# Kernel tuning notes

Measured on AMD Instinct MI355X. Metric: run time of the kernel, lower is better.

Reference implementation:

```python
import jax, jax.numpy as jnp
import numpy as np

N = 8192
K = 30


def setup_inputs() -> dict:
    key = jax.random.key(0)
    k1, k2, k3 = jax.random.split(key, 3)
    estimate = jax.random.normal(k1, (N, K), dtype=jnp.float32)
    event_time = jax.random.uniform(k2, (N,), dtype=jnp.float32) * 30.0
    event = (jax.random.uniform(k3, (N,)) < 0.7).astype(jnp.float32)
    target = jnp.stack([event_time, event], axis=1)  # [N, 2]
    intervals = (jnp.arange(K, dtype=jnp.float32) + 0.5)  # midpoints per init_kwargs
    return {"estimate": estimate, "target": target, "intervals": intervals}


def reference(estimate, target, intervals):
    event_time = target[:, 0]
    event = target[:, 1] != 0
    # hazard -> survival via exclusive cumprod (pad with 1 at the front)
    hazard = jax.nn.sigmoid(estimate)                       # [N, K]
    surv = jnp.cumprod(1.0 - hazard, axis=-1)               # inclusive cumprod
    surv_prev = jnp.concatenate(
        [jnp.ones_like(surv[..., :1]), surv[..., :-1]], axis=-1
    )                                                       # S(t_{k-1}), exclusive
    pdf = hazard * surv_prev                                # [N, K]
    mrl = jnp.sum(intervals * pdf, axis=-1)                 # [N]
    # comparable pairs: i has an event and t_i < t_j
    comparable = (event_time[:, None] < event_time[None, :]) & event[:, None]
    diff = mrl[:, None] - mrl[None, :]                      # [N, N]
    cnt = jnp.sum(comparable).astype(diff.dtype)
    return jnp.sum(jnp.where(comparable, diff, 0.0)) / cnt
```

## Files before the change

kernel.cpp:

```cpp
#include <hip/hip_runtime.h>
#include <math.h>

constexpr int N     = 8192;
constexpr int K     = 30;
constexpr int TPB   = 1024;
constexpr int NI    = N / TPB;
constexpr int NJ    = 32;
constexpr int JSPAN = N / NJ;
constexpr int NBLK  = NI * NJ;
constexpr int MB    = 128;
constexpr int FTPB  = 256;


__global__ void mrl_kernel(const float* __restrict__ est,
                           const float* __restrict__ intervals,
                           float* __restrict__ mrl) {
    __shared__ float s_est[MB * K];

    const int tid  = threadIdx.x;
    const int row0 = blockIdx.x * MB;

    const float2* src = (const float2*)(est + (size_t)row0 * K);
    float2* dst = (float2*)s_est;
#pragma unroll
    for (int t = 0; t < K / 2; ++t)
        dst[t * MB + tid] = src[t * MB + tid];
    __syncthreads();

    const float* e = s_est + tid * K;
    double sp = 1.0, m = 0.0;
#pragma unroll
    for (int k = 0; k < K; ++k) {
        float hf = 1.0f / (1.0f + __expf(-e[k]));
        double h = (double)hf;
        m += (double)intervals[k] * h * sp;
        sp *= (1.0 - h);
    }
    mrl[row0 + tid] = (float)m;
}

__global__ void pair_kernel(const float* __restrict__ target,
                            const float* __restrict__ mrl,
                            double* __restrict__ pnum,
                            int* __restrict__ pcnt) {
    __shared__ __align__(16) float s_t[JSPAN];
    __shared__ __align__(16) float s_m[JSPAN];
    __shared__ double r_num[TPB];
    __shared__ int    r_cnt[TPB];

    const int tid = threadIdx.x;
    const int bid = blockIdx.x;
    const int ib  = bid >> 5;
    const int js  = bid & (NJ - 1);
    const int i   = ib * TPB + tid;

    const float2 ti2 = ((const float2*)target)[i];
    const float  ti  = ti2.x;
    const bool   ei  = (ti2.y != 0.0f);
    const float  mi  = mrl[i];

    if (tid < JSPAN) {
        const int j = js * JSPAN + tid;
        s_t[tid] = ((const float2*)target)[j].x;
        s_m[tid] = mrl[j];
    }
    __syncthreads();

    const float4* s_t4 = (const float4*)s_t;
    const float4* s_m4 = (const float4*)s_m;

    double smj = 0.0;
    int c0 = 0, c1 = 0, c2 = 0, c3 = 0;

#pragma unroll
    for (int ch = 0; ch < JSPAN / 64; ++ch) {
        float a0 = 0.f, a1 = 0.f, a2 = 0.f, a3 = 0.f;
#pragma unroll
        for (int q = 0; q < 16; ++q) {
            const int jj4 = ch * 16 + q;
            float4 tv = s_t4[jj4];
            float4 mv = s_m4[jj4];
            bool b0 = ti < tv.x, b1 = ti < tv.y, b2 = ti < tv.z, b3 = ti < tv.w;
            c0 += b0; a0 += b0 ? mv.x : 0.0f;
            c1 += b1; a1 += b1 ? mv.y : 0.0f;
            c2 += b2; a2 += b2 ? mv.z : 0.0f;
            c3 += b3; a3 += b3 ? mv.w : 0.0f;
        }
        smj += (double)((a0 + a1) + (a2 + a3));
    }

    const int cnt = (c0 + c1) + (c2 + c3);
    r_num[tid] = ei ? ((double)cnt * (double)mi - smj) : 0.0;
    r_cnt[tid] = ei ? cnt : 0;
    __syncthreads();
    for (int s = TPB / 2; s > 0; s >>= 1) {
        if (tid < s) {
            r_num[tid] += r_num[tid + s];
            r_cnt[tid] += r_cnt[tid + s];
        }
        __syncthreads();
    }
    if (tid == 0) {
        pnum[bid] = r_num[0];
        pcnt[bid] = r_cnt[0];
    }
}

__global__ void final_kernel(const double* __restrict__ pnum,
                             const int* __restrict__ pcnt,
                             float* __restrict__ out) {
    __shared__ double r_num[FTPB];
    __shared__ int    r_cnt[FTPB];
    const int tid = threadIdx.x;
    r_num[tid] = pnum[tid];
    r_cnt[tid] = pcnt[tid];
    __syncthreads();
    for (int s = FTPB / 2; s > 0; s >>= 1) {
        if (tid < s) {
            r_num[tid] += r_num[tid + s];
            r_cnt[tid] += r_cnt[tid + s];
        }
        __syncthreads();
    }
    if (tid == 0) out[0] = (float)(r_num[0] / (double)r_cnt[0]);
}

extern "C" void kernel_launch(void* const* d_in, const int* in_sizes, int n_in,
                              void* d_out, int out_size, void* d_ws, size_t ws_size,
                              hipStream_t stream) {
    const float* est       = (const float*)d_in[0];
    const float* target    = (const float*)d_in[1];
    const float* intervals = (const float*)d_in[2];
    float* out = (float*)d_out;

    float*  mrl  = (float*)d_ws;
    double* pnum = (double*)((char*)d_ws + 32768);
    int*    pcnt = (int*)((char*)d_ws + 34816);

    mrl_kernel<<<N / MB, MB, 0, stream>>>(est, intervals, mrl);
    pair_kernel<<<NBLK, TPB, 0, stream>>>(target, mrl, pnum, pcnt);
    final_kernel<<<1, FTPB, 0, stream>>>(pnum, pcnt, out);
}
```

Before: 20.52 us.

## Replace all-pairs comparison with time-binned prefix sums over sorted buckets

Replaces the O(N^2) pairwise comparable-pair kernel with a histogram-based approach. A single-block kernel buckets event times into 1024 bins, builds prefix counts and prefix mrl sums per bin, and keeps a bucket-sorted index list. Each row then gets its count and sum from the bins strictly above its own, plus an explicit scan within its own bin. This cuts the quadratic work to near-linear work, at the cost of a serial single-block indexing kernel with many barriers and an extra launch. Rows that pile into one bin would make that bin's scan slow.

Measured after the change: 35.84 us. +74.6%, slower.

```diff
diff --git a/kernel.cpp b/kernel.cpp
--- a/kernel.cpp
+++ b/kernel.cpp
@@ -3,14 +3,17 @@
 
 constexpr int N     = 8192;
 constexpr int K     = 30;
-constexpr int TPB   = 1024;
-constexpr int NI    = N / TPB;
-constexpr int NJ    = 32;
-constexpr int JSPAN = N / NJ;
-constexpr int NBLK  = NI * NJ;
+constexpr int NBINS = 1024;
 constexpr int MB    = 128;
-constexpr int FTPB  = 256;
-
+constexpr int GB    = 256;
+constexpr int GBLK  = N / GB;
+
+
+__device__ __forceinline__ int bin_of(float t) {
+    int b = (int)(t * (float)(NBINS / 30.0));
+    b = b < 0 ? 0 : b;
+    return b > NBINS - 1 ? NBINS - 1 : b;
+}
 
 __global__ void mrl_kernel(const float* __restrict__ est,
                            const float* __restrict__ intervals,
@@ -39,61 +42,116 @@
     mrl[row0 + tid] = (float)m;
 }
 
-__global__ void pair_kernel(const float* __restrict__ target,
-                            const float* __restrict__ mrl,
-                            double* __restrict__ pnum,
-                            int* __restrict__ pcnt) {
-    __shared__ __align__(16) float s_t[JSPAN];
-    __shared__ __align__(16) float s_m[JSPAN];
-    __shared__ double r_num[TPB];
-    __shared__ int    r_cnt[TPB];
+__global__ void __launch_bounds__(NBINS)
+index_kernel(const float* __restrict__ target,
+             const float* __restrict__ mrlv,
+             unsigned int* __restrict__ g_incl_cnt,
+             double* __restrict__ g_incl_sum,
+             unsigned short* __restrict__ g_sidx) {
+    __shared__ unsigned int   hist[NBINS];
+    __shared__ unsigned int   incl[NBINS];
+    __shared__ unsigned int   fill[NBINS];
+    __shared__ double         dA[NBINS];
+    __shared__ unsigned short sidx[N];
 
     const int tid = threadIdx.x;
-    const int bid = blockIdx.x;
-    const int ib  = bid >> 5;
-    const int js  = bid & (NJ - 1);
-    const int i   = ib * TPB + tid;
-
-    const float2 ti2 = ((const float2*)target)[i];
-    const float  ti  = ti2.x;
-    const bool   ei  = (ti2.y != 0.0f);
-    const float  mi  = mrl[i];
-
-    if (tid < JSPAN) {
-        const int j = js * JSPAN + tid;
-        s_t[tid] = ((const float2*)target)[j].x;
-        s_m[tid] = mrl[j];
-    }
-    __syncthreads();
-
-    const float4* s_t4 = (const float4*)s_t;
-    const float4* s_m4 = (const float4*)s_m;
-
-    double smj = 0.0;
-    int c0 = 0, c1 = 0, c2 = 0, c3 = 0;
-
-#pragma unroll
-    for (int ch = 0; ch < JSPAN / 64; ++ch) {
-        float a0 = 0.f, a1 = 0.f, a2 = 0.f, a3 = 0.f;
-#pragma unroll
-        for (int q = 0; q < 16; ++q) {
-            const int jj4 = ch * 16 + q;
-            float4 tv = s_t4[jj4];
-            float4 mv = s_m4[jj4];
-            bool b0 = ti < tv.x, b1 = ti < tv.y, b2 = ti < tv.z, b3 = ti < tv.w;
-            c0 += b0; a0 += b0 ? mv.x : 0.0f;
-            c1 += b1; a1 += b1 ? mv.y : 0.0f;
-            c2 += b2; a2 += b2 ? mv.z : 0.0f;
-            c3 += b3; a3 += b3 ? mv.w : 0.0f;
+
+    hist[tid] = 0u;
+    fill[tid] = 0u;
+    __syncthreads();
+
+#pragma unroll
+    for (int r = 0; r < N / NBINS; ++r) {
+        const int i = r * NBINS + tid;
+        atomicAdd(&hist[bin_of(target[2 * i])], 1u);
+    }
+    __syncthreads();
+
+    incl[tid] = hist[tid];
+    __syncthreads();
+    for (int off = 1; off < NBINS; off <<= 1) {
+        const unsigned int add = (tid >= off) ? incl[tid - off] : 0u;
+        __syncthreads();
+        incl[tid] += add;
+        __syncthreads();
+    }
+
+#pragma unroll
+    for (int r = 0; r < N / NBINS; ++r) {
+        const int i = r * NBINS + tid;
+        const int b = bin_of(target[2 * i]);
+        const unsigned int start = (b > 0) ? incl[b - 1] : 0u;
+        const unsigned int slot  = atomicAdd(&fill[b], 1u);
+        sidx[start + slot] = (unsigned short)i;
+    }
+    __syncthreads();
+
+    {
+        const int b = tid;
+        const int s = (b > 0) ? (int)incl[b - 1] : 0;
+        const int e = (int)incl[b];
+        for (int p = s + 1; p < e; ++p) {
+            const unsigned short v = sidx[p];
+            int q = p - 1;
+            while (q >= s && sidx[q] > v) { sidx[q + 1] = sidx[q]; --q; }
+            sidx[q + 1] = v;
         }
-        smj += (double)((a0 + a1) + (a2 + a3));
-    }
-
-    const int cnt = (c0 + c1) + (c2 + c3);
-    r_num[tid] = ei ? ((double)cnt * (double)mi - smj) : 0.0;
-    r_cnt[tid] = ei ? cnt : 0;
-    __syncthreads();
-    for (int s = TPB / 2; s > 0; s >>= 1) {
+        double bs = 0.0;
+        for (int p = s; p < e; ++p)
+            bs += (double)mrlv[sidx[p]];
+        dA[b] = bs;
+    }
+    __syncthreads();
+
+    for (int off = 1; off < NBINS; off <<= 1) {
+        const double add = (tid >= off) ? dA[tid - off] : 0.0;
+        __syncthreads();
+        dA[tid] += add;
+        __syncthreads();
+    }
+
+    g_incl_cnt[tid] = incl[tid];
+    g_incl_sum[tid] = dA[tid];
+#pragma unroll
+    for (int r = 0; r < N / NBINS; ++r)
+        g_sidx[r * NBINS + tid] = sidx[r * NBINS + tid];
+}
+
+__global__ void finalize_kernel(const float* __restrict__ target,
+                                const float* __restrict__ mrlv,
+                                const unsigned int* __restrict__ incl_cnt,
+                                const double* __restrict__ incl_sum,
+                                const unsigned short* __restrict__ sidx,
+                                double* __restrict__ pnum,
+                                int* __restrict__ pcnt) {
+    __shared__ double r_num[GB];
+    __shared__ int    r_cnt[GB];
+
+    const int tid = threadIdx.x;
+    const int i   = blockIdx.x * GB + tid;
+
+    const float2 tv = ((const float2*)target)[i];
+    const float  ti = tv.x;
+    const bool   ev = (tv.y != 0.0f);
+    const float  mi = mrlv[i];
+
+    const int b = bin_of(ti);
+    const unsigned int endo   = incl_cnt[b];
+    const unsigned int starto = (b > 0) ? incl_cnt[b - 1] : 0u;
+
+    double S = incl_sum[NBINS - 1] - incl_sum[b];
+    int    c = N - (int)endo;
+
+    for (unsigned int p = starto; p < endo; ++p) {
+        const int   j  = sidx[p];
+        const float tj = target[2 * j];
+        if (tj > ti) { ++c; S += (double)mrlv[j]; }
+    }
+
+    r_num[tid] = ev ? ((double)c * (double)mi - S) : 0.0;
+    r_cnt[tid] = ev ? c : 0;
+    __syncthreads();
+    for (int s = GB / 2; s > 0; s >>= 1) {
         if (tid < s) {
             r_num[tid] += r_num[tid + s];
             r_cnt[tid] += r_cnt[tid + s];
@@ -101,28 +159,22 @@
         __syncthreads();
     }
     if (tid == 0) {
-        pnum[bid] = r_num[0];
-        pcnt[bid] = r_cnt[0];
-    }
-}
-
-__global__ void final_kernel(const double* __restrict__ pnum,
-                             const int* __restrict__ pcnt,
-                             float* __restrict__ out) {
-    __shared__ double r_num[FTPB];
-    __shared__ int    r_cnt[FTPB];
-    const int tid = threadIdx.x;
-    r_num[tid] = pnum[tid];
-    r_cnt[tid] = pcnt[tid];
-    __syncthreads();
-    for (int s = FTPB / 2; s > 0; s >>= 1) {
-        if (tid < s) {
-            r_num[tid] += r_num[tid + s];
-            r_cnt[tid] += r_cnt[tid + s];
-        }
-        __syncthreads();
-    }
-    if (tid == 0) out[0] = (float)(r_num[0] / (double)r_cnt[0]);
+        pnum[blockIdx.x] = r_num[0];
+        pcnt[blockIdx.x] = r_cnt[0];
+    }
+}
+
+__global__ void out_kernel(const double* __restrict__ pnum,
+                           const int* __restrict__ pcnt,
+                           float* __restrict__ out) {
+    double n = 0.0;
+    double c = 0.0;
+#pragma unroll
+    for (int p = 0; p < GBLK; ++p) {
+        n += pnum[p];
+        c += (double)pcnt[p];
+    }
+    out[0] = (float)(n / c);
 }
 
 extern "C" void kernel_launch(void* const* d_in, const int* in_sizes, int n_in,
@@ -133,11 +185,16 @@
     const float* intervals = (const float*)d_in[2];
     float* out = (float*)d_out;
 
-    float*  mrl  = (float*)d_ws;
-    double* pnum = (double*)((char*)d_ws + 32768);
-    int*    pcnt = (int*)((char*)d_ws + 34816);
+    float*          mrl      = (float*)d_ws;
+    unsigned int*   incl_cnt = (unsigned int*)((char*)d_ws + 32768);
+    double*         incl_sum = (double*)((char*)d_ws + 36864);
+    unsigned short* sidx     = (unsigned short*)((char*)d_ws + 45056);
+    double*         pnum     = (double*)((char*)d_ws + 61440);
+    int*            pcnt     = (int*)((char*)d_ws + 61696);
 
     mrl_kernel<<<N / MB, MB, 0, stream>>>(est, intervals, mrl);
-    pair_kernel<<<NBLK, TPB, 0, stream>>>(target, mrl, pnum, pcnt);
-    final_kernel<<<1, FTPB, 0, stream>>>(pnum, pcnt, out);
-}
+    index_kernel<<<1, NBINS, 0, stream>>>(target, mrl, incl_cnt, incl_sum, sidx);
+    finalize_kernel<<<GBLK, GB, 0, stream>>>(target, mrl, incl_cnt, incl_sum,
+                                             sidx, pnum, pcnt);
+    out_kernel<<<1, 1, 0, stream>>>(pnum, pcnt, out);
+}
```
